# Optimization experiments

Measured on AMD Instinct MI355X. Metric: run time of the kernel, lower is better.

Reference implementation:

```python
import jax, jax.numpy as jnp
import numpy as np

B, N, M = 8, 8192, 1024
C1, C2 = 256, 512
C_IN, C_MID, C_OUT = 768, 256, 256  # mlp = [768, 256, 256]
EPS_BN = 1e-5
EPS_W = 1e-8


def setup_inputs() -> dict:
    key = jax.random.key(0)
    ks = jax.random.split(key, 10)
    inp = {
        "unknown": jax.random.uniform(ks[0], (B, N, 3), dtype=jnp.float32),
        "known": jax.random.uniform(ks[1], (B, M, 3), dtype=jnp.float32),
        "unknow_feats": jax.random.normal(ks[2], (B, C1, N), dtype=jnp.float32),
        "known_feats": jax.random.normal(ks[3], (B, C2, M), dtype=jnp.float32),
        # conv1d (kernel=1) weights, bias-free (followed by BN), per create_convblock1d
        "W1": jax.random.normal(ks[4], (C_MID, C_IN), dtype=jnp.float32) * (1.0 / np.sqrt(C_IN)),
        "g1": jnp.ones((C_MID,), jnp.float32),
        "b1": jnp.zeros((C_MID,), jnp.float32),
        "W2": jax.random.normal(ks[5], (C_OUT, C_MID), dtype=jnp.float32) * (1.0 / np.sqrt(C_MID)),
        "g2": jnp.ones((C_OUT,), jnp.float32),
        "b2": jnp.zeros((C_OUT,), jnp.float32),
    }
    return inp


def _three_interpolation(unknown, known, known_feats):
    # squared pairwise distances (B, N, M), as in pointnet2 three_nn CUDA kernel
    d2 = jnp.sum((unknown[:, :, None, :] - known[:, None, :, :]) ** 2, axis=-1)
    neg_d, idx = jax.lax.top_k(-d2, 3)            # (B, N, 3)
    dist = -neg_d
    w = 1.0 / (dist + EPS_W)
    w = w / jnp.sum(w, axis=-1, keepdims=True)    # (B, N, 3)
    gathered = jax.vmap(lambda f, i: f[:, i])(known_feats, idx)  # (B, C2, N, 3)
    return jnp.einsum("bcnk,bnk->bcn", gathered, w)              # (B, C2, N)


def _conv_bn_relu(x, W, g, b):
    # 1x1 conv1d (no bias) + BatchNorm1d (training-mode stats) + ReLU
    y = jnp.einsum("oc,bcn->bon", W, x)
    mean = jnp.mean(y, axis=(0, 2), keepdims=True)
    var = jnp.var(y, axis=(0, 2), keepdims=True)
    y = (y - mean) * jax.lax.rsqrt(var + EPS_BN)
    y = y * g[None, :, None] + b[None, :, None]
    return jax.nn.relu(y)


def reference(unknown, known, unknow_feats, known_feats, W1, g1, b1, W2, g2, b2):
    interp = _three_interpolation(unknown, known, known_feats)   # (B, C2, N)
    new_features = jnp.concatenate([unknow_feats, interp], axis=1)  # (B, C1+C2, N)
    h = _conv_bn_relu(new_features, W1, g1, b1)
    out = _conv_bn_relu(h, W2, g2, b2)
    return out  # (B, C_OUT, N)
```

## Files before the change

### kernel.cpp

```cpp
#include <hip/hip_runtime.h>

#define B_    8
#define N_    8192
#define M_    1024
#define C1_   256
#define C2_   512
#define CIN_  768
#define CMID_ 256
#define COUT_ 256

typedef __attribute__((ext_vector_type(8))) __bf16 bf16x8;
typedef __attribute__((ext_vector_type(4))) float f32x4;
typedef __attribute__((ext_vector_type(4))) unsigned short u16x4;
typedef __attribute__((ext_vector_type(8))) unsigned short u16x8;

__device__ __forceinline__ unsigned short f2bf(float f) {
  union { float f; unsigned u; } v; v.f = f;
  unsigned r = v.u + 0x7FFFu + ((v.u >> 16) & 1u);
  return (unsigned short)(r >> 16);
}
__device__ __forceinline__ float bf2f(unsigned short h) {
  union { unsigned u; float f; } v; v.u = ((unsigned)h) << 16; return v.f;
}

__device__ __forceinline__ void gload16(const void* g, void* l) {
  __builtin_amdgcn_global_load_lds((const __attribute__((address_space(1))) unsigned int*)g,
                                   (__attribute__((address_space(3))) unsigned int*)l, 16, 0, 0);
}


__global__ void k_cast(const float* __restrict__ in, unsigned short* __restrict__ out, int n) {
  int i = blockIdx.x * 256 + threadIdx.x;
  if (i < n) out[i] = f2bf(in[i]);
}

__global__ void k_tr_kf(const float* __restrict__ in, float* __restrict__ out) {
  __shared__ float t[32][33];
  int b = blockIdx.z;
  int c0 = blockIdx.x * 32, m0 = blockIdx.y * 32;
  int tx = threadIdx.x, ty = threadIdx.y;
  const float* ip = in + ((size_t)b * C2_ + c0) * M_ + m0;
#pragma unroll
  for (int i = 0; i < 32; i += 8) t[ty + i][tx] = ip[(size_t)(ty + i) * M_ + tx];
  __syncthreads();
  float* op = out + ((size_t)b * M_ + m0) * C2_ + c0;
#pragma unroll
  for (int i = 0; i < 32; i += 8) op[(size_t)(ty + i) * C2_ + tx] = t[tx][ty + i];
}

__global__ void k_tr_uf(const float* __restrict__ in, unsigned short* __restrict__ out) {
  __shared__ float t[32][33];
  int b = blockIdx.z;
  int c0 = blockIdx.x * 32, n0 = blockIdx.y * 32;
  int tx = threadIdx.x, ty = threadIdx.y;
  const float* ip = in + ((size_t)b * C1_ + c0) * N_ + n0;
#pragma unroll
  for (int i = 0; i < 32; i += 8) t[ty + i][tx] = ip[(size_t)(ty + i) * N_ + tx];
  __syncthreads();
  unsigned short* op = out + ((size_t)b * N_ + n0) * CIN_ + c0;
#pragma unroll
  for (int i = 0; i < 32; i += 8) op[(size_t)(ty + i) * CIN_ + tx] = f2bf(t[tx][ty + i]);
}


__device__ __forceinline__ void ins3(float db, int ib, float& d0, int& i0,
                                     float& d1, int& i1, float& d2, int& i2) {
  if (db < d2 || (db == d2 && ib < i2)) {
    if (db < d1 || (db == d1 && ib < i1)) {
      d2 = d1; i2 = i1;
      if (db < d0 || (db == d0 && ib < i0)) { d1 = d0; i1 = i0; d0 = db; i0 = ib; }
      else                                  { d1 = db; i1 = ib; }
    } else { d2 = db; i2 = ib; }
  }
}

__global__ __launch_bounds__(256) void k_three_nn(const float* __restrict__ unknown,
                                                  const float* __restrict__ known,
                                                  int* __restrict__ idx, float* __restrict__ wgt) {
  __shared__ __align__(16) float kpts[M_][4];
  int b = blockIdx.x >> 8;
  int n0 = (blockIdx.x & 255) << 5;
  for (int i = threadIdx.x; i < M_; i += 256) {
    const float* kp = known + ((size_t)b * M_ + i) * 3;
    kpts[i][0] = kp[0]; kpts[i][1] = kp[1]; kpts[i][2] = kp[2];
  }
  __syncthreads();
  const int l = threadIdx.x & 63;
  const int j = l & 7;
  const int q = ((threadIdx.x >> 6) << 3) + (l >> 3);
  const int n = n0 + q;
  const float* up = unknown + ((size_t)b * N_ + n) * 3;
  float ux = up[0], uy = up[1], uz = up[2];
  float d0 = 1e30f, d1 = 1e30f, d2v = 1e30f;
  int i0 = 0, i1 = 0, i2 = 0;
  for (int t = 0; t < 128; ++t) {
    int i = t * 8 + j;
    f32x4 p = *(const f32x4*)kpts[i];
    float dx = __fsub_rn(ux, p[0]);
    float dy = __fsub_rn(uy, p[1]);
    float dz = __fsub_rn(uz, p[2]);
    float d = __fadd_rn(__fadd_rn(__fmul_rn(dx, dx), __fmul_rn(dy, dy)), __fmul_rn(dz, dz));
    if (d < d2v) {
      if (d < d1) {
        if (d < d0) { d2v = d1; i2 = i1; d1 = d0; i1 = i0; d0 = d; i0 = i; }
        else        { d2v = d1; i2 = i1; d1 = d;  i1 = i; }
      } else        { d2v = d;  i2 = i; }
    }
  }
#pragma unroll
  for (int m = 1; m <= 4; m <<= 1) {
    float e0 = __shfl_xor(d0, m), e1 = __shfl_xor(d1, m), e2 = __shfl_xor(d2v, m);
    int   f0 = __shfl_xor(i0, m), f1 = __shfl_xor(i1, m), f2 = __shfl_xor(i2, m);
    ins3(e0, f0, d0, i0, d1, i1, d2v, i2);
    ins3(e1, f1, d0, i0, d1, i1, d2v, i2);
    ins3(e2, f2, d0, i0, d1, i1, d2v, i2);
  }
  if (j == 0) {
    float w0 = 1.f / (d0 + 1e-8f), w1 = 1.f / (d1 + 1e-8f), w2 = 1.f / (d2v + 1e-8f);
    float s = w0 + w1 + w2;
    size_t base = ((size_t)b * N_ + n) * 3;
    idx[base] = i0; idx[base + 1] = i1; idx[base + 2] = i2;
    wgt[base] = w0 / s; wgt[base + 1] = w1 / s; wgt[base + 2] = w2 / s;
  }
}

__global__ __launch_bounds__(256) void k_interp(const float* __restrict__ kft, const int* __restrict__ idx,
                                                const float* __restrict__ wgt, unsigned short* __restrict__ xt) {
  int pb = blockIdx.x * 8 + (threadIdx.x >> 5);
  int lane = threadIdx.x & 31;
  int b = pb >> 13;
  size_t t3 = (size_t)pb * 3;
  int i0 = idx[t3], i1 = idx[t3 + 1], i2 = idx[t3 + 2];
  float w0 = wgt[t3], w1 = wgt[t3 + 1], w2 = wgt[t3 + 2];
  const f32x4* f0 = (const f32x4*)(kft + ((size_t)b * M_ + i0) * C2_);
  const f32x4* f1 = (const f32x4*)(kft + ((size_t)b * M_ + i1) * C2_);
  const f32x4* f2 = (const f32x4*)(kft + ((size_t)b * M_ + i2) * C2_);
  unsigned short* o = xt + (size_t)pb * CIN_ + C1_;
#pragma unroll
  for (int k = 0; k < 4; ++k) {
    int c4 = lane + 32 * k;
    f32x4 a = f0[c4], bb = f1[c4], cc = f2[c4];
    u16x4 r;
#pragma unroll
    for (int e = 0; e < 4; ++e) r[e] = f2bf(w0 * a[e] + w1 * bb[e] + w2 * cc[e]);
    *(u16x4*)(o + 4 * c4) = r;
  }
}


template <int K, int EPI, bool BN>
__global__ __launch_bounds__(256) void gemm_bt(const unsigned short* __restrict__ A,
                                               const unsigned short* __restrict__ Bm,
                                               unsigned short* __restrict__ C,
                                               float* __restrict__ psum, float* __restrict__ psq,
                                               const float* __restrict__ scale,
                                               const float* __restrict__ shift) {
  __shared__ __align__(16) char lds[65536];
  const int tid = threadIdx.x;
  const int l = tid & 63;
  const int wv = tid >> 6;
  const int wr = wv >> 1, wc = wv & 1;
  const int b = blockIdx.z;
  const int o0 = blockIdx.y * 128;
  const int n0 = blockIdx.x * 128;
  const char* Ab = (const char*)A + (size_t)o0 * (K * 2);
  const char* Bb = (const char*)Bm + ((size_t)b * N_ + n0) * (K * 2);

  f32x4 zero = {0.f, 0.f, 0.f, 0.f};
  f32x4 acc[4][4];
#pragma unroll
  for (int i = 0; i < 4; ++i)
#pragma unroll
    for (int j = 0; j < 4; ++j) acc[i][j] = zero;

  const int grow = wv * 32 + (l >> 3);
  const int gcol = (((l & 7) ^ (l >> 3)) * 16);
  int srow[4], scol[4];
#pragma unroll
  for (int i = 0; i < 4; ++i) { int q = tid + i * 256; srow[i] = q >> 3; scol[i] = (q & 7) * 16; }

  auto bnwrite = [&](bf16x8* rb, int ktv, char* dstbase) {
#pragma unroll
    for (int i = 0; i < 4; ++i) {
      u16x8 v = *(u16x8*)&rb[i];
      int c0 = ktv * 64 + (scol[i] >> 1);
      f32x4 sa = *(const f32x4*)(scale + c0), sb = *(const f32x4*)(scale + c0 + 4);
      f32x4 ha = *(const f32x4*)(shift + c0), hb = *(const f32x4*)(shift + c0 + 4);
      u16x8 r;
#pragma unroll
      for (int e = 0; e < 4; ++e) {
        r[e]     = f2bf(fmaxf(bf2f(v[e])     * sa[e] + ha[e], 0.f));
        r[e + 4] = f2bf(fmaxf(bf2f(v[e + 4]) * sb[e] + hb[e], 0.f));
      }
      *(u16x8*)(dstbase + srow[i] * 128 + (scol[i] ^ ((srow[i] & 7) << 4))) = r;
    }
  };

  if (BN) {
    bf16x8 rb0[4];
#pragma unroll
    for (int i = 0; i < 4; ++i)
      rb0[i] = *(const bf16x8*)(Bb + (size_t)srow[i] * (K * 2) + scol[i]);
#pragma unroll
    for (int i = 0; i < 4; ++i)
      gload16(Ab + (size_t)(grow + i * 8) * (K * 2) + gcol, lds + wv * 4096 + i * 1024);
    bnwrite(rb0, 0, lds + 16384);
  } else {
#pragma unroll
    for (int i = 0; i < 4; ++i) {
      int r = grow + i * 8;
      gload16(Ab + (size_t)r * (K * 2) + gcol, lds + wv * 4096 + i * 1024);
      gload16(Bb + (size_t)r * (K * 2) + gcol, lds + 16384 + wv * 4096 + i * 1024);
    }
  }
  __syncthreads();

  const int NK = K / 64;
  int cur = 0;
  for (int kt = 0; kt < NK; ++kt) {
    const bool haveNext = (kt + 1 < NK);
    bf16x8 rb2[4];
    if (haveNext) {
      char* nb = lds + (cur ^ 1) * 32768;
      if (BN) {
        const char* Bk = Bb + (size_t)(kt + 1) * 128;
#pragma unroll
        for (int i = 0; i < 4; ++i)
          rb2[i] = *(const bf16x8*)(Bk + (size_t)srow[i] * (K * 2) + scol[i]);
#pragma unroll
        for (int i = 0; i < 4; ++i)
          gload16(Ab + (size_t)(grow + i * 8) * (K * 2) + (kt + 1) * 128 + gcol,
                  nb + wv * 4096 + i * 1024);
      } else {
#pragma unroll
        for (int i = 0; i < 4; ++i) {
          int r = grow + i * 8;
          gload16(Ab + (size_t)r * (K * 2) + (kt + 1) * 128 + gcol, nb + wv * 4096 + i * 1024);
          gload16(Bb + (size_t)r * (K * 2) + (kt + 1) * 128 + gcol, nb + 16384 + wv * 4096 + i * 1024);
        }
      }
    }
    const char* base = lds + cur * 32768;
#pragma unroll
    for (int kk = 0; kk < 2; ++kk) {
      bf16x8 af[4], bfr[4];
#pragma unroll
      for (int mi = 0; mi < 4; ++mi) {
        int row = wr * 64 + mi * 16 + (l & 15);
        int cb = (kk * 64 + ((l >> 4) * 16)) ^ ((row & 7) << 4);
        af[mi] = *(const bf16x8*)(base + row * 128 + cb);
      }
#pragma unroll
      for (int ni = 0; ni < 4; ++ni) {
        int row = wc * 64 + ni * 16 + (l & 15);
        int cb = (kk * 64 + ((l >> 4) * 16)) ^ ((row & 7) << 4);
        bfr[ni] = *(const bf16x8*)(base + 16384 + row * 128 + cb);
      }
#pragma unroll
      for (int mi = 0; mi < 4; ++mi)
#pragma unroll
        for (int ni = 0; ni < 4; ++ni)
          acc[mi][ni] = __builtin_amdgcn_mfma_f32_16x16x32_bf16(af[mi], bfr[ni], acc[mi][ni], 0, 0, 0);
    }
    if (BN && haveNext) bnwrite(rb2, kt + 1, lds + (cur ^ 1) * 32768 + 16384);
    __syncthreads();
    cur ^= 1;
  }

  const int slot = (blockIdx.z * 64 + blockIdx.x) * 2 + wc;
#pragma unroll
  for (int mi = 0; mi < 4; ++mi) {
    float s[4] = {0.f, 0.f, 0.f, 0.f}, q[4] = {0.f, 0.f, 0.f, 0.f};
#pragma unroll
    for (int ni = 0; ni < 4; ++ni)
#pragma unroll
      for (int r = 0; r < 4; ++r) { float v = acc[mi][ni][r]; s[r] += v; q[r] = fmaf(v, v, q[r]); }
#pragma unroll
    for (int m = 1; m <= 8; m <<= 1)
#pragma unroll
      for (int r = 0; r < 4; ++r) { s[r] += __shfl_xor(s[r], m); q[r] += __shfl_xor(q[r], m); }
    if ((l & 15) == 0) {
      int o = o0 + wr * 64 + mi * 16 + ((l >> 4) << 2);
#pragma unroll
      for (int r = 0; r < 4; ++r) {
        psum[(size_t)(o + r) * 1024 + slot] = s[r];
        psq [(size_t)(o + r) * 1024 + slot] = q[r];
      }
    }
  }

  unsigned short* t16 = (unsigned short*)lds;
#pragma unroll
  for (int mi = 0; mi < 4; ++mi) {
    int ol = wr * 64 + mi * 16 + ((l >> 4) << 2);
#pragma unroll
    for (int ni = 0; ni < 4; ++ni) {
      int nl = wc * 64 + ni * 16 + (l & 15);
#pragma unroll
      for (int r = 0; r < 4; ++r) {
        unsigned short v = f2bf(acc[mi][ni][r]);
        if (EPI == 0) t16[nl * 144 + ol + r] = v;
        else          t16[(ol + r) * 144 + nl] = v;
      }
    }
  }
  __syncthreads();
#pragma unroll
  for (int t = 0; t < 8; ++t) {
    int row = wv * 32 + (l >> 4) + t * 4;
    u16x8 v = *(const u16x8*)(t16 + row * 144 + (l & 15) * 8);
    if (EPI == 0)
      *(u16x8*)(C + ((size_t)b * N_ + n0 + row) * 256 + o0 + (l & 15) * 8) = v;
    else
      *(u16x8*)(C + ((size_t)b * 256 + o0 + row) * N_ + n0 + (l & 15) * 8) = v;
  }
}


__global__ __launch_bounds__(256) void k_finalize(const float* __restrict__ psum,
                                                  const float* __restrict__ psq,
                                                  const float* __restrict__ g,
                                                  const float* __restrict__ bb,
                                                  float* __restrict__ scale,
                                                  float* __restrict__ shift) {
  int c = blockIdx.x;
  const float* ps = psum + (size_t)c * 1024;
  const float* pq = psq + (size_t)c * 1024;
  float s = 0.f, q = 0.f;
#pragma unroll
  for (int k = 0; k < 4; ++k) { s += ps[threadIdx.x + 256 * k]; q += pq[threadIdx.x + 256 * k]; }
#pragma unroll
  for (int off = 32; off; off >>= 1) { s += __shfl_down(s, off); q += __shfl_down(q, off); }
  __shared__ float rs[4], rq[4];
  if ((threadIdx.x & 63) == 0) { rs[threadIdx.x >> 6] = s; rq[threadIdx.x >> 6] = q; }
  __syncthreads();
  if (threadIdx.x == 0) {
    float S = rs[0] + rs[1] + rs[2] + rs[3];
    float Q = rq[0] + rq[1] + rq[2] + rq[3];
    const float inv_n = 1.f / 65536.f;
    float mean = S * inv_n;
    float var = Q * inv_n - mean * mean;
    float rstd = rsqrtf(var + 1e-5f);
    float sc = g[c] * rstd;
    scale[c] = sc;
    shift[c] = bb[c] - mean * sc;
  }
}

__global__ void k_bnrelu_out(const unsigned short* __restrict__ y, const float* __restrict__ scale,
                             const float* __restrict__ shift, float* __restrict__ out) {
  size_t i = ((size_t)blockIdx.x * 256 + threadIdx.x) * 4;
  int c = (int)((i >> 13) & 255);
  float sc = scale[c], sh = shift[c];
  u16x4 v = *(const u16x4*)(y + i);
  f32x4 o;
#pragma unroll
  for (int k = 0; k < 4; ++k) o[k] = fmaxf(bf2f(v[k]) * sc + sh, 0.f);
  *(f32x4*)(out + i) = o;
}


extern "C" void kernel_launch(void* const* d_in, const int* in_sizes, int n_in,
                              void* d_out, int out_size, void* d_ws, size_t ws_size,
                              hipStream_t stream) {
  const float* unknown = (const float*)d_in[0];
  const float* known   = (const float*)d_in[1];
  const float* uf      = (const float*)d_in[2];
  const float* kf      = (const float*)d_in[3];
  const float* W1      = (const float*)d_in[4];
  const float* g1      = (const float*)d_in[5];
  const float* b1      = (const float*)d_in[6];
  const float* W2      = (const float*)d_in[7];
  const float* g2      = (const float*)d_in[8];
  const float* b2      = (const float*)d_in[9];
  float* out = (float*)d_out;

  char* ws = (char*)d_ws;
  unsigned short* xt  = (unsigned short*)(ws);
  unsigned short* y1  = (unsigned short*)(ws + 100663296);
  unsigned short* y2  = (unsigned short*)(ws + 134217728);
  float*          kft = (float*)(ws + 167772160);
  float*          psum = (float*)(ws + 167772160);
  float*          psq  = (float*)(ws + 168820736);
  unsigned short* w1b = (unsigned short*)(ws + 184549376);
  unsigned short* w2b = (unsigned short*)(ws + 184942592);
  int*            idx = (int*)(ws + 185073664);
  float*          wgt = (float*)(ws + 185860096);
  float*          st  = (float*)(ws + 186646528);
  float *sc1 = st, *sh1 = st + 256, *sc2 = st + 512, *sh2 = st + 768;

  k_cast<<<768, 256, 0, stream>>>(W1, w1b, CMID_ * CIN_);
  k_cast<<<256, 256, 0, stream>>>(W2, w2b, COUT_ * CMID_);
  k_tr_kf<<<dim3(16, 32, B_), dim3(32, 8), 0, stream>>>(kf, kft);
  k_tr_uf<<<dim3(8, 256, B_), dim3(32, 8), 0, stream>>>(uf, xt);
  k_three_nn<<<B_ * 256, 256, 0, stream>>>(unknown, known, idx, wgt);
  k_interp<<<B_ * N_ / 8, 256, 0, stream>>>(kft, idx, wgt, xt);
  gemm_bt<CIN_, 0, false><<<dim3(64, 2, B_), 256, 0, stream>>>(w1b, xt, y1, psum, psq, nullptr, nullptr);
  k_finalize<<<256, 256, 0, stream>>>(psum, psq, g1, b1, sc1, sh1);
  gemm_bt<CMID_, 1, true><<<dim3(64, 2, B_), 256, 0, stream>>>(w2b, y1, y2, psum, psq, sc1, sh1);
  k_finalize<<<256, 256, 0, stream>>>(psum, psq, g2, b2, sc2, sh2);
  k_bnrelu_out<<<16384, 256, 0, stream>>>(y2, sc2, sh2, out);
}
```

Measured before the change: 197.2 us.

## Halve GEMM K-tile to shrink LDS and raise occupancy, cache BN params in LDS

The bf16 MFMA GEMM now uses a K-tile of 32 instead of 64, which cuts the double-buffered LDS footprint from 64KB to about 36KB. It adds launch bounds of 4 blocks per CU and a new XOR swizzle suited to 64-byte rows. BN scale and shift vectors are staged once into LDS, replacing per-tile global vector loads. The goal is more resident blocks to hide memory latency, at the cost of twice as many loop iterations and barriers, plus possible register pressure from the launch-bound cap.

```diff
diff --git a/kernel.cpp b/kernel.cpp
--- a/kernel.cpp
+++ b/kernel.cpp
@@ -149,13 +149,15 @@
 
 
 template <int K, int EPI, bool BN>
-__global__ __launch_bounds__(256) void gemm_bt(const unsigned short* __restrict__ A,
-                                               const unsigned short* __restrict__ Bm,
-                                               unsigned short* __restrict__ C,
-                                               float* __restrict__ psum, float* __restrict__ psq,
-                                               const float* __restrict__ scale,
-                                               const float* __restrict__ shift) {
-  __shared__ __align__(16) char lds[65536];
+__global__ __launch_bounds__(256, 4) void gemm_bt(const unsigned short* __restrict__ A,
+                                                  const unsigned short* __restrict__ Bm,
+                                                  unsigned short* __restrict__ C,
+                                                  float* __restrict__ psum, float* __restrict__ psq,
+                                                  const float* __restrict__ scale,
+                                                  const float* __restrict__ shift) {
+  __shared__ __align__(16) char lds[36864];
+  float* lsc = (float*)(lds + 32768);
+  float* lsh = (float*)(lds + 33792);
   const int tid = threadIdx.x;
   const int l = tid & 63;
   const int wv = tid >> 6;
@@ -166,103 +168,94 @@
   const char* Ab = (const char*)A + (size_t)o0 * (K * 2);
   const char* Bb = (const char*)Bm + ((size_t)b * N_ + n0) * (K * 2);
 
-  f32x4 zero = {0.f, 0.f, 0.f, 0.f};
+  if (BN) {
+    lsc[tid] = scale[tid]; lsh[tid] = shift[tid];
+    __syncthreads();
+  }
+
   f32x4 acc[4][4];
 #pragma unroll
   for (int i = 0; i < 4; ++i)
 #pragma unroll
-    for (int j = 0; j < 4; ++j) acc[i][j] = zero;
-
-  const int grow = wv * 32 + (l >> 3);
-  const int gcol = (((l & 7) ^ (l >> 3)) * 16);
-  int srow[4], scol[4];
-#pragma unroll
-  for (int i = 0; i < 4; ++i) { int q = tid + i * 256; srow[i] = q >> 3; scol[i] = (q & 7) * 16; }
-
-  auto bnwrite = [&](bf16x8* rb, int ktv, char* dstbase) {
-#pragma unroll
-    for (int i = 0; i < 4; ++i) {
+    for (int j = 0; j < 4; ++j) acc[i][j] = f32x4{0.f, 0.f, 0.f, 0.f};
+
+  const int grow = wv * 32 + (l >> 2);
+  const int gcol = ((l & 3) ^ ((l >> 3) & 3)) * 16;
+  int srow[2], sg[2];
+#pragma unroll
+  for (int i = 0; i < 2; ++i) { int q = tid + i * 256; srow[i] = q >> 2; sg[i] = q & 3; }
+
+  auto issueA = [&](int kt, char* buf) {
+#pragma unroll
+    for (int i = 0; i < 2; ++i)
+      gload16(Ab + (size_t)(grow + i * 16) * (K * 2) + kt * 64 + gcol,
+              buf + wv * 2048 + i * 1024);
+  };
+  auto issueB = [&](int kt, char* buf) {
+#pragma unroll
+    for (int i = 0; i < 2; ++i)
+      gload16(Bb + (size_t)(grow + i * 16) * (K * 2) + kt * 64 + gcol,
+              buf + 8192 + wv * 2048 + i * 1024);
+  };
+  auto loadBreg = [&](bf16x8* rb, int kt) {
+#pragma unroll
+    for (int i = 0; i < 2; ++i)
+      rb[i] = *(const bf16x8*)(Bb + (size_t)srow[i] * (K * 2) + kt * 64 + sg[i] * 16);
+  };
+  auto bnwrite = [&](bf16x8* rb, int kt, char* buf) {
+#pragma unroll
+    for (int i = 0; i < 2; ++i) {
       u16x8 v = *(u16x8*)&rb[i];
-      int c0 = ktv * 64 + (scol[i] >> 1);
-      f32x4 sa = *(const f32x4*)(scale + c0), sb = *(const f32x4*)(scale + c0 + 4);
-      f32x4 ha = *(const f32x4*)(shift + c0), hb = *(const f32x4*)(shift + c0 + 4);
+      int c0 = kt * 32 + sg[i] * 8;
       u16x8 r;
 #pragma unroll
-      for (int e = 0; e < 4; ++e) {
-        r[e]     = f2bf(fmaxf(bf2f(v[e])     * sa[e] + ha[e], 0.f));
-        r[e + 4] = f2bf(fmaxf(bf2f(v[e + 4]) * sb[e] + hb[e], 0.f));
-      }
-      *(u16x8*)(dstbase + srow[i] * 128 + (scol[i] ^ ((srow[i] & 7) << 4))) = r;
+      for (int e = 0; e < 8; ++e)
+        r[e] = f2bf(fmaxf(bf2f(v[e]) * lsc[c0 + e] + lsh[c0 + e], 0.f));
+      *(u16x8*)(buf + 8192 + srow[i] * 64 + (sg[i] ^ ((srow[i] >> 1) & 3)) * 16) = r;
     }
   };
 
   if (BN) {
-    bf16x8 rb0[4];
-#pragma unroll
-    for (int i = 0; i < 4; ++i)
-      rb0[i] = *(const bf16x8*)(Bb + (size_t)srow[i] * (K * 2) + scol[i]);
-#pragma unroll
-    for (int i = 0; i < 4; ++i)
-      gload16(Ab + (size_t)(grow + i * 8) * (K * 2) + gcol, lds + wv * 4096 + i * 1024);
-    bnwrite(rb0, 0, lds + 16384);
+    bf16x8 rb0[2];
+    loadBreg(rb0, 0);
+    issueA(0, lds);
+    bnwrite(rb0, 0, lds);
   } else {
-#pragma unroll
-    for (int i = 0; i < 4; ++i) {
-      int r = grow + i * 8;
-      gload16(Ab + (size_t)r * (K * 2) + gcol, lds + wv * 4096 + i * 1024);
-      gload16(Bb + (size_t)r * (K * 2) + gcol, lds + 16384 + wv * 4096 + i * 1024);
-    }
-  }
-  __syncthreads();
-
-  const int NK = K / 64;
+    issueA(0, lds);
+    issueB(0, lds);
+  }
+  __syncthreads();
+
+  const int NK = K / 32;
   int cur = 0;
   for (int kt = 0; kt < NK; ++kt) {
     const bool haveNext = (kt + 1 < NK);
-    bf16x8 rb2[4];
+    char* nb = lds + (cur ^ 1) * 16384;
+    bf16x8 rb2[2];
     if (haveNext) {
-      char* nb = lds + (cur ^ 1) * 32768;
-      if (BN) {
-        const char* Bk = Bb + (size_t)(kt + 1) * 128;
-#pragma unroll
-        for (int i = 0; i < 4; ++i)
-          rb2[i] = *(const bf16x8*)(Bk + (size_t)srow[i] * (K * 2) + scol[i]);
-#pragma unroll
-        for (int i = 0; i < 4; ++i)
-          gload16(Ab + (size_t)(grow + i * 8) * (K * 2) + (kt + 1) * 128 + gcol,
-                  nb + wv * 4096 + i * 1024);
-      } else {
-#pragma unroll
-        for (int i = 0; i < 4; ++i) {
-          int r = grow + i * 8;
-          gload16(Ab + (size_t)r * (K * 2) + (kt + 1) * 128 + gcol, nb + wv * 4096 + i * 1024);
-          gload16(Bb + (size_t)r * (K * 2) + (kt + 1) * 128 + gcol, nb + 16384 + wv * 4096 + i * 1024);
-        }
-      }
-    }
-    const char* base = lds + cur * 32768;
-#pragma unroll
-    for (int kk = 0; kk < 2; ++kk) {
-      bf16x8 af[4], bfr[4];
-#pragma unroll
-      for (int mi = 0; mi < 4; ++mi) {
-        int row = wr * 64 + mi * 16 + (l & 15);
-        int cb = (kk * 64 + ((l >> 4) * 16)) ^ ((row & 7) << 4);
-        af[mi] = *(const bf16x8*)(base + row * 128 + cb);
-      }
-#pragma unroll
-      for (int ni = 0; ni < 4; ++ni) {
-        int row = wc * 64 + ni * 16 + (l & 15);
-        int cb = (kk * 64 + ((l >> 4) * 16)) ^ ((row & 7) << 4);
-        bfr[ni] = *(const bf16x8*)(base + 16384 + row * 128 + cb);
-      }
-#pragma unroll
-      for (int mi = 0; mi < 4; ++mi)
-#pragma unroll
-        for (int ni = 0; ni < 4; ++ni)
-          acc[mi][ni] = __builtin_amdgcn_mfma_f32_16x16x32_bf16(af[mi], bfr[ni], acc[mi][ni], 0, 0, 0);
-    }
-    if (BN && haveNext) bnwrite(rb2, kt + 1, lds + (cur ^ 1) * 32768 + 16384);
+      if (BN) { loadBreg(rb2, kt + 1); issueA(kt + 1, nb); }
+      else    { issueA(kt + 1, nb); issueB(kt + 1, nb); }
+    }
+    const char* base = lds + cur * 16384;
+    bf16x8 af[4], bfr[4];
+#pragma unroll
+    for (int mi = 0; mi < 4; ++mi) {
+      int row = wr * 64 + mi * 16 + (l & 15);
+      int g = (l >> 4) ^ ((row >> 1) & 3);
+      af[mi] = *(const bf16x8*)(base + row * 64 + g * 16);
+    }
+#pragma unroll
+    for (int ni = 0; ni < 4; ++ni) {
+      int row = wc * 64 + ni * 16 + (l & 15);
+      int g = (l >> 4) ^ ((row >> 1) & 3);
+      bfr[ni] = *(const bf16x8*)(base + 8192 + row * 64 + g * 16);
+    }
+#pragma unroll
+    for (int mi = 0; mi < 4; ++mi)
+#pragma unroll
+      for (int ni = 0; ni < 4; ++ni)
+        acc[mi][ni] = __builtin_amdgcn_mfma_f32_16x16x32_bf16(af[mi], bfr[ni], acc[mi][ni], 0, 0, 0);
+    if (BN && haveNext) bnwrite(rb2, kt + 1, nb);
     __syncthreads();
     cur ^= 1;
   }
```

Result: slower. 205.8 us (+4.4%).
